# Kernel tuning notes

Measured on AMD Instinct MI355X. Metric: run time of the kernel, lower is better.

Reference implementation:

```python
import jax, jax.numpy as jnp
import numpy as np

H, L, N1, N2, N3 = 256, 141, 9, 34, 98
B, S = 64, 512

def setup_inputs() -> dict:
    key = jax.random.key(0)
    cnt = [0]
    def nrm(shape, s=0.05):
        cnt[0] += 1
        return jax.random.normal(jax.random.fold_in(key, cnt[0]), shape, jnp.float32) * s
    d = {}
    d['inputs'] = jax.random.randint(jax.random.fold_in(key, 1000), (B, S), 0, 30522)
    d['text_hidden'] = nrm((B, S, 768), 1.0)
    d['label_encoding'] = nrm((L, H), 1.0)
    d['w12'] = (jax.random.uniform(jax.random.fold_in(key, 1001), (N1, N2)) < 0.3).astype(jnp.float32)
    d['w23'] = (jax.random.uniform(jax.random.fold_in(key, 1002), (N2, N3)) < 0.3).astype(jnp.float32)
    d['fre12'] = jax.random.uniform(jax.random.fold_in(key, 1003), (N1, N2), jnp.float32)
    d['fre23'] = jax.random.uniform(jax.random.fold_in(key, 1004), (N2, N3), jnp.float32)
    for name in ['wi1', 'wf1', 'wo1', 'wu1', 'wi2', 'wf2', 'wo2', 'wu2']:
        d[name + '_W'] = nrm((H, H)); d[name + '_b'] = nrm((H,))
    for name in ['ui1', 'uf1', 'uo1', 'uu1', 'ui2', 'uf2', 'uo2', 'uu2']:
        d[name + '_W'] = nrm((H, H))
    d['mix_W'] = nrm((3 * H, H)); d['mix_b'] = nrm((H,))
    d['tt_W'] = nrm((768, H)); d['tt_b'] = nrm((H,))
    d['A'] = nrm((L, L)); d['Wp'] = nrm((H, H))
    d['out_W'] = nrm((L * H, L)); d['out_b'] = nrm((L,))
    return d

def reference(inputs, text_hidden, label_encoding, w12, w23, fre12, fre23,
              wi1_W, wi1_b, wf1_W, wf1_b, wo1_W, wo1_b, wu1_W, wu1_b,
              wi2_W, wi2_b, wf2_W, wf2_b, wo2_W, wo2_b, wu2_W, wu2_b,
              ui1_W, uf1_W, uo1_W, uu1_W, ui2_W, uf2_W, uo2_W, uu2_W,
              mix_W, mix_b, tt_W, tt_b, A, Wp, out_W, out_b):
    sig, tanh = jax.nn.sigmoid, jnp.tanh
    v1 = label_encoding[:N1]          # [N1,H]
    v2 = label_encoding[N1:N1 + N2]   # [N2,H]
    v3 = label_encoding[N1 + N2:]     # [N3,H]
    w21, w32 = w12.T, w23.T
    # --- top-down tree-LSTM (suffix 1) ---
    i11 = sig(v1 @ wi1_W + wi1_b); o11 = sig(v1 @ wo1_W + wo1_b); u11 = tanh(v1 @ wu1_W + wu1_b)
    c11 = i11 * u11; h11 = o11 * tanh(c11)
    h21t = w21 @ h11
    i21 = sig(v2 @ wi1_W + wi1_b + h21t @ ui1_W)
    f21 = sig(v2 @ wf1_W + wf1_b + h21t @ uf1_W)
    o21 = sig(v2 @ wo1_W + wo1_b + h21t @ uo1_W)
    u21 = tanh(v2 @ wu1_W + wu1_b + h21t @ uu1_W)
    c21 = i21 * u21 + f21 * (w21 @ c11); h21 = o21 * tanh(c21)
    h31t = w32 @ h21
    i31 = sig(v3 @ wi1_W + wi1_b + h31t @ ui1_W)
    f31 = sig(v3 @ wf1_W + wf1_b + h31t @ uf1_W)
    o31 = sig(v3 @ wo1_W + wo1_b + h31t @ uo1_W)
    u31 = tanh(v3 @ wu1_W + wu1_b + h31t @ uu1_W)
    c31 = i31 * u31 + f31 * (w32 @ c21); h31 = o31 * tanh(c31)
    # --- bottom-up tree-LSTM (suffix 2) ---
    i32 = sig(v3 @ wi2_W + wi2_b); o32 = sig(v3 @ wo2_W + wo2_b); u32 = tanh(v3 @ wu2_W + wu2_b)
    c32 = i32 * u32; h32 = o32 * tanh(c32)
    h22t = fre23 @ h32
    i22 = sig(v2 @ wi2_W + wi2_b + h22t @ ui2_W)
    f22 = sig((w32 @ v2) @ wf2_W + wf2_b + h32 @ uf2_W)   # [N3,H]
    o22 = sig(v2 @ wo2_W + wo2_b + h22t @ uo2_W)
    u22 = tanh(v2 @ wu2_W + wu2_b + h22t @ uu2_W)
    c22 = i22 * u22 + w23 @ (f22 * c32); h22 = o22 * tanh(c22)
    h12t = fre12 @ h22
    i12 = sig(v1 @ wi2_W + wi2_b + h12t @ ui2_W)
    f12 = sig((w21 @ v1) @ wf2_W + wf2_b + h22 @ uf2_W)   # [N2,H]
    o12 = sig(v1 @ wo2_W + wo2_b + h12t @ uo2_W)
    u12 = tanh(v1 @ wu2_W + wu2_b + h12t @ uu2_W)
    c12 = i12 * u12 + w12 @ (f12 * c22); h12 = o12 * tanh(c12)
    h1 = jnp.concatenate([h11, h12], axis=1)
    h2 = jnp.concatenate([h21, h22], axis=1)
    h3 = jnp.concatenate([h31, h32], axis=1)
    le = jnp.concatenate([h1, h2, h3], axis=0)            # [L,2H]
    temp = jax.nn.relu(A @ label_encoding @ Wp)           # [L,H]
    le = jnp.concatenate([le, temp], axis=1) @ mix_W + mix_b  # [L,H]
    # --- masked cross-attention pooling over text ---
    text = tanh(text_hidden @ tt_W + tt_b)                # [B,S,H]
    att = jnp.einsum('lh,bsh->bls', le, text)             # [B,L,S]
    pad = jnp.where((inputs == 0) | (inputs == 101) | (inputs == 102), -jnp.inf, 0.0).astype(text.dtype)
    att = jax.nn.softmax(att + pad[:, None, :], axis=2)
    features = jnp.einsum('bls,bsh->blh', att, text).reshape(inputs.shape[0], -1)  # [B,L*H]
    return sig(features @ out_W + out_b)                  # [B,L]
```

## Files before the change

kernel.cpp:

```cpp
#include <hip/hip_runtime.h>
#include <math.h>

static constexpr int H = 256, L = 141, N1 = 9, N2 = 34, N3 = 98;
static constexpr int B = 64, S = 512;

typedef __attribute__((ext_vector_type(8))) _Float16 f16x8;
typedef __attribute__((ext_vector_type(4))) float f32x4;

__device__ inline unsigned short f2h(float x) {
    _Float16 h = (_Float16)x;
    return __builtin_bit_cast(unsigned short, h);
}
__device__ inline float sigf(float x) { return 1.f / (1.f + __expf(-x)); }

__device__ inline void gload_lds16(const void* g, void* l) {
    __builtin_amdgcn_global_load_lds(
        (const __attribute__((address_space(1))) void*)g,
        (__attribute__((address_space(3))) void*)l, 16, 0, 0);
}

template<int EPI, bool CONVA, int IM>
__global__ __launch_bounds__(256) void gemm_mfma(
    const void* __restrict__ Aptr, int lda, long strA,
    const unsigned short* __restrict__ Bp, int ldb, long strB,
    float* __restrict__ C, int ldc, long strC,
    int M, int N, int K,
    const float* __restrict__ bias,
    const int* __restrict__ tokens,
    unsigned short* __restrict__ outH,
    unsigned short* __restrict__ outHT,
    int kChunk)
{
    __shared__ unsigned short A_s[32 * IM * 32];
    __shared__ unsigned short B_s[128 * 32];
    __shared__ unsigned short T[EPI == 1 ? 128 * 64 : 1];
    const int tid  = threadIdx.x;
    const int wave = tid >> 6, lane = tid & 63;
    const int quad = lane >> 4, l16 = lane & 15;
    const int bz = blockIdx.z;
    const int m0 = blockIdx.y * (32 * IM), n0 = blockIdx.x * 128;
    const int wm = (wave & 1) * (16 * IM), wn = (wave >> 1) * 64;

    long aBase, bBase;
    int kBeg, kEnd;
    if (EPI == 4) { aBase = 0; bBase = 0; kBeg = bz * kChunk; kEnd = kBeg + kChunk; }
    else { aBase = (long)bz * strA; bBase = (long)bz * strB; kBeg = 0; kEnd = K; }

    f32x4 acc[IM][4] = {};

    for (int k0 = kBeg; k0 < kEnd; k0 += 32) {
        if (CONVA) {
            const float* Af = (const float*)Aptr + aBase;
            #pragma unroll
            for (int it = 0; it < IM; it++) {
                int idx = it * 256 + tid;
                int row = idx >> 3, col4 = idx & 7;
                int gm = m0 + row; if (gm > M - 1) gm = M - 1;
                float4 v = *(const float4*)(Af + (long)gm * lda + k0 + col4 * 4);
                unsigned int p0 = f2h(v.x) | ((unsigned int)f2h(v.y) << 16);
                unsigned int p1 = f2h(v.z) | ((unsigned int)f2h(v.w) << 16);
                *(uint2*)&A_s[row * 32 + col4 * 4] = make_uint2(p0, p1);
            }
        } else {
            const unsigned short* Ab = (const unsigned short*)Aptr + aBase;
            #pragma unroll
            for (int t = 0; t < IM / 2; t++) {
                int rowb = wave * (8 * IM) + t * 16;
                int gm = m0 + rowb + (lane >> 2); if (gm > M - 1) gm = M - 1;
                gload_lds16(Ab + (long)gm * lda + k0 + (lane & 3) * 8,
                            &A_s[rowb * 32]);
            }
        }
        #pragma unroll
        for (int t = 0; t < 2; t++) {
            int rowb = wave * 32 + t * 16;
            int gn = n0 + rowb + (lane >> 2); if (gn > N - 1) gn = N - 1;
            gload_lds16(Bp + bBase + (long)gn * ldb + k0 + (lane & 3) * 8,
                        &B_s[rowb * 32]);
        }
        __syncthreads();
        f16x8 a[IM], b[4];
        #pragma unroll
        for (int i = 0; i < IM; i++)
            a[i] = *(const f16x8*)&A_s[(wm + i * 16 + l16) * 32 + quad * 8];
        #pragma unroll
        for (int j = 0; j < 4; j++)
            b[j] = *(const f16x8*)&B_s[(wn + j * 16 + l16) * 32 + quad * 8];
        #pragma unroll
        for (int i = 0; i < IM; i++)
            #pragma unroll
            for (int j = 0; j < 4; j++)
                acc[i][j] = __builtin_amdgcn_mfma_f32_16x16x32_f16(
                    a[i], b[j], acc[i][j], 0, 0, 0);
        __syncthreads();
    }

    #pragma unroll
    for (int i = 0; i < IM; i++) {
        #pragma unroll
        for (int j = 0; j < 4; j++) {
            #pragma unroll
            for (int r = 0; r < 4; r++) {
                int ml = wm + i * 16 + quad * 4 + r;
                int nl = wn + j * 16 + l16;
                int gm = m0 + ml, gn = n0 + nl;
                if (gm >= M || gn >= N) continue;
                float v = acc[i][j][r];
                if (EPI == 1) {
                    v = tanhf(v + bias[gn]);
                    unsigned short hv = f2h(v);
                    outH[(long)gm * ldc + gn] = hv;
                    T[nl * 64 + ml] = hv;
                } else if (EPI == 2) {
                    int tok = tokens[(long)bz * 512 + gn];
                    if (tok == 0 || tok == 101 || tok == 102) v -= 1e30f;
                    C[(long)bz * strC + (long)gm * ldc + gn] = v;
                } else if (EPI == 3) {
                    outH[(long)bz * strC + (long)gm * ldc + gn] = f2h(v);
                } else {
                    C[(long)bz * strC + (long)gm * ldc + gn] = v;
                }
            }
        }
    }
    if (EPI == 1) {
        __syncthreads();
        int bb = m0 >> 9, s0 = m0 & 511;
        int rr = tid >> 1, half = tid & 1;
        const uint4* srcp = (const uint4*)&T[rr * 64 + half * 32];
        uint4* dstp = (uint4*)&outHT[((long)bb * 256 + n0 + rr) * 512 + s0 + half * 32];
        dstp[0] = srcp[0]; dstp[1] = srcp[1]; dstp[2] = srcp[2]; dstp[3] = srcp[3];
    }
}

__global__ __launch_bounds__(256) void transp_t64(
    const float* __restrict__ src, unsigned short* __restrict__ dst,
    int R, int C)
{
    __shared__ unsigned short T[64 * 65];
    const int tid = threadIdx.x;
    const int r0 = blockIdx.x * 64, c0 = blockIdx.y * 64;
    #pragma unroll
    for (int p = 0; p < 16; p++) {
        int lin = p * 256 + tid;
        int r = lin >> 6, c = lin & 63;
        int gc = c0 + c;
        float v = (gc < C) ? src[(long)(r0 + r) * C + gc] : 0.f;
        T[c * 65 + r] = f2h(v);
    }
    __syncthreads();
    #pragma unroll
    for (int p = 0; p < 16; p++) {
        int lin = p * 256 + tid;
        int c = lin >> 6, r = lin & 63;
        if (c0 + c < C)
            dst[(long)(c0 + c) * R + r0 + r] = T[c * 65 + r];
    }
}

__global__ __launch_bounds__(256) void gate_pre(
    const float* __restrict__ le,
    const float* W0, const float* W1, const float* W2, const float* W3,
    const float* W4, const float* W5, const float* W6,
    const float* b0, const float* b1, const float* b2, const float* b3,
    const float* b4, const float* b5, const float* b6,
    float* __restrict__ G)
{
    __shared__ float ls[256];
    __shared__ float red[256];
    const int j = blockIdx.x >> 2, x = blockIdx.x & 3, m = blockIdx.y;
    const int tid = threadIdx.x, nl = tid & 63, ks = tid >> 6, n = x * 64 + nl;
    ls[tid] = le[(long)m * 256 + tid];
    __syncthreads();
    const float *W, *bb;
    switch (j) {
        case 0: W = W0; bb = b0; break;  case 1: W = W1; bb = b1; break;
        case 2: W = W2; bb = b2; break;  case 3: W = W3; bb = b3; break;
        case 4: W = W4; bb = b4; break;  case 5: W = W5; bb = b5; break;
        default: W = W6; bb = b6;
    }
    float a0 = 0, a1 = 0, a2 = 0, a3 = 0;
    for (int k = ks; k + 12 < 256; k += 16) {
        long o = (long)k * 256 + n;
        a0 += ls[k] * W[o];        a1 += ls[k + 4] * W[o + 1024];
        a2 += ls[k + 8] * W[o + 2048]; a3 += ls[k + 12] * W[o + 3072];
    }
    red[tid] = a0 + a1 + a2 + a3;
    __syncthreads();
    if (ks == 0)
        G[((long)j * 141 + m) * 256 + n] =
            red[nl] + red[64 + nl] + red[128 + nl] + red[192 + nl] + bb[n];
}

__global__ __launch_bounds__(256) void pre2(
    const float* __restrict__ A, const float* __restrict__ le,
    const float* __restrict__ w23, const float* __restrict__ w12,
    const float* __restrict__ Wp, const float* __restrict__ wf2_W,
    float* __restrict__ tmpP, float* __restrict__ wv2f, float* __restrict__ wv1f)
{
    __shared__ float cs[141];
    __shared__ float t[256];
    __shared__ float red[256];
    const int x = blockIdx.x, y = blockIdx.y;
    const int tid = threadIdx.x, nl = tid & 63, ks = tid >> 6, n = x * 64 + nl;
    int job, m, K1;
    if (y < 141)      { job = 0; m = y;       K1 = 141; }
    else if (y < 239) { job = 1; m = y - 141; K1 = 34; }
    else              { job = 2; m = y - 239; K1 = 9; }
    if (tid < K1)
        cs[tid] = (job == 0) ? A[(long)m * 141 + tid]
                : (job == 1) ? w23[(long)tid * 98 + m]
                             : w12[(long)tid * 34 + m];
    __syncthreads();
    const float* s1 = (job == 1) ? le + 9 * 256 : le;
    float acc = 0;
    #pragma unroll 4
    for (int k = 0; k < K1; k++) acc += cs[k] * s1[(long)k * 256 + tid];
    t[tid] = acc;
    __syncthreads();
    const float* W = (job == 0) ? Wp : wf2_W;
    float a0 = 0, a1 = 0, a2 = 0, a3 = 0;
    for (int k = ks; k + 12 < 256; k += 16) {
        long o = (long)k * 256 + n;
        a0 += t[k] * W[o];        a1 += t[k + 4] * W[o + 1024];
        a2 += t[k + 8] * W[o + 2048]; a3 += t[k + 12] * W[o + 3072];
    }
    red[tid] = a0 + a1 + a2 + a3;
    __syncthreads();
    if (ks == 0) {
        float tot = red[nl] + red[64 + nl] + red[128 + nl] + red[192 + nl];
        if (job == 0)      tmpP[(long)m * 256 + n] = fmaxf(tot, 0.f);
        else if (job == 1) wv2f[(long)m * 256 + n] = tot;
        else               wv1f[(long)m * 256 + n] = tot;
    }
}

__global__ __launch_bounds__(256) void ew1(
    const float* __restrict__ G, float* __restrict__ h11, float* __restrict__ c11,
    float* __restrict__ h32, float* __restrict__ c32)
{
    int y = blockIdx.x, n = threadIdx.x;
    if (y < 9) {
        int m = y;
        float iv = sigf(G[(0L * 141 + m) * 256 + n]);
        float ov = sigf(G[(2L * 141 + m) * 256 + n]);
        float uv = tanhf(G[(3L * 141 + m) * 256 + n]);
        float cv = iv * uv;
        c11[m * 256 + n] = cv; h11[m * 256 + n] = ov * tanhf(cv);
    } else {
        int r = y - 9, grow = 43 + r;
        float iv = sigf(G[(4L * 141 + grow) * 256 + n]);
        float ov = sigf(G[(5L * 141 + grow) * 256 + n]);
        float uv = tanhf(G[(6L * 141 + grow) * 256 + n]);
        float cv = iv * uv;
        c32[r * 256 + n] = cv; h32[r * 256 + n] = ov * tanhf(cv);
    }
}

__global__ __launch_bounds__(256) void chain_mm(int phase,
    const float* __restrict__ w12, const float* __restrict__ w23,
    const float* __restrict__ fre23, const float* __restrict__ fre12,
    const float* __restrict__ h11, const float* __restrict__ c11,
    const float* __restrict__ h32,
    const float* __restrict__ h21, const float* __restrict__ c21,
    const float* __restrict__ h22,
    const float* __restrict__ wv2f, const float* __restrict__ wv1f,
    const float* __restrict__ wf2_b, const float* __restrict__ uf2_W,
    const float* __restrict__ c32, const float* __restrict__ c22,
    float* __restrict__ h21t, float* __restrict__ c21p,
    float* __restrict__ h22t, float* __restrict__ fcb,
    float* __restrict__ h31t, float* __restrict__ c31p,
    float* __restrict__ h12t, float* __restrict__ fc2b)
{
    __shared__ float cs[256];
    __shared__ float red[256];
    const int x = blockIdx.x, y = blockIdx.y;
    const int tid = threadIdx.x, nl = tid & 63, ks = tid >> 6, n = x * 64 + nl;
    int job, m;
    if (phase == 0) {
        if (y < 34)       { job = 0; m = y; }
        else if (y < 68)  { job = 1; m = y - 34; }
        else if (y < 102) { job = 2; m = y - 68; }
        else              { job = 3; m = y - 102; }
    } else {
        if (y < 98)       { job = 0; m = y; }
        else if (y < 196) { job = 1; m = y - 98; }
        else if (y < 205) { job = 2; m = y - 196; }
        else              { job = 3; m = y - 205; }
    }
    if (job < 3) {
        int K; const float* src; float* dst;
        if (phase == 0) {
            K = (job == 2) ? 98 : 9;
            src = (job == 0) ? h11 : (job == 1) ? c11 : h32;
            dst = (job == 0) ? h21t : (job == 1) ? c21p : h22t;
            if (tid < K)
                cs[tid] = (job == 2) ? fre23[(long)m * 98 + tid]
                                     : w12[(long)tid * 34 + m];
        } else {
            K = 34;
            src = (job == 0) ? h21 : (job == 1) ? c21 : h22;
            dst = (job == 0) ? h31t : (job == 1) ? c31p : h12t;
            if (tid < K)
                cs[tid] = (job == 2) ? fre12[(long)m * 34 + tid]
                                     : w23[(long)tid * 98 + m];
        }
        __syncthreads();
        float a0 = 0;
        for (int k = ks; k < K; k += 4) a0 += cs[k] * src[(long)k * 256 + n];
        red[tid] = a0;
        __syncthreads();
        if (ks == 0)
            dst[(long)m * 256 + n] = red[nl] + red[64 + nl] + red[128 + nl] + red[192 + nl];
    } else {
        const float* row = (phase == 0) ? h32 + m * 256 : h22 + m * 256;
        const float* pre = (phase == 0) ? wv2f : wv1f;
        const float* cm  = (phase == 0) ? c32 : c22;
        float* dst       = (phase == 0) ? fcb : fc2b;
        cs[tid] = row[tid];
        __syncthreads();
        float a0 = 0, a1 = 0, a2 = 0, a3 = 0;
        for (int k = ks; k + 12 < 256; k += 16) {
            long o = (long)k * 256 + n;
            a0 += cs[k] * uf2_W[o];        a1 += cs[k + 4] * uf2_W[o + 1024];
            a2 += cs[k + 8] * uf2_W[o + 2048]; a3 += cs[k + 12] * uf2_W[o + 3072];
        }
        red[tid] = a0 + a1 + a2 + a3;
        __syncthreads();
        if (ks == 0) {
            float tot = red[nl] + red[64 + nl] + red[128 + nl] + red[192 + nl]
                      + pre[(long)m * 256 + n] + wf2_b[n];
            dst[(long)m * 256 + n] = sigf(tot) * cm[(long)m * 256 + n];
        }
    }
}

__global__ __launch_bounds__(256) void lstm_fused(int phase,
    const float* __restrict__ G,
    const float* __restrict__ h21t, const float* __restrict__ c21p,
    const float* __restrict__ h22t, const float* __restrict__ fcb,
    const float* __restrict__ h31t, const float* __restrict__ c31p,
    const float* __restrict__ h12t, const float* __restrict__ fc2b,
    const float* __restrict__ w23, const float* __restrict__ w12,
    const float* __restrict__ ui1, const float* __restrict__ uf1,
    const float* __restrict__ uo1, const float* __restrict__ uu1,
    const float* __restrict__ ui2, const float* __restrict__ uo2,
    const float* __restrict__ uu2,
    float* __restrict__ h21, float* __restrict__ c21,
    float* __restrict__ h22, float* __restrict__ c22,
    float* __restrict__ h31, float* __restrict__ h12)
{
    __shared__ float hs[256];
    __shared__ float cs[128];
    __shared__ float red[1024];
    const int x = blockIdx.x, y = blockIdx.y;
    const int tid = threadIdx.x, nl = tid & 63, ks = tid >> 6, n = x * 64 + nl;
    bool modef; int m, grow, Kx = 0;
    const float *hrow, *U0, *U1, *U2, *U3 = nullptr, *Sx = nullptr, *cmod = nullptr;
    float *ho, *co = nullptr;
    if (phase == 0) {
        if (y < 34) { modef = true;  m = y;      grow = 9 + m;  hrow = h21t;
                      U0 = ui1; U1 = uf1; U2 = uo1; U3 = uu1; cmod = c21p; ho = h21; co = c21; }
        else        { modef = false; m = y - 34; grow = 9 + m;  hrow = h22t;
                      U0 = ui2; U1 = uo2; U2 = uu2; Sx = fcb; Kx = 98; ho = h22; co = c22;
                      if (tid < 98) cs[tid] = w23[(long)m * 98 + tid]; }
    } else {
        if (y < 98) { modef = true;  m = y;      grow = 43 + m; hrow = h31t;
                      U0 = ui1; U1 = uf1; U2 = uo1; U3 = uu1; cmod = c31p; ho = h31; co = nullptr; }
        else        { modef = false; m = y - 98; grow = m;      hrow = h12t;
                      U0 = ui2; U1 = uo2; U2 = uu2; Sx = fc2b; Kx = 34; ho = h12; co = nullptr;
                      if (tid < 34) cs[tid] = w12[(long)m * 34 + tid]; }
    }
    hs[tid] = hrow[(long)m * 256 + tid];
    __syncthreads();
    float a0 = 0, a1 = 0, a2 = 0, a3 = 0;
    if (modef) {
        for (int k = ks; k < 256; k += 4) {
            float xv = hs[k]; long o = (long)k * 256 + n;
            a0 += xv * U0[o]; a1 += xv * U1[o]; a2 += xv * U2[o]; a3 += xv * U3[o];
        }
    } else {
        for (int k = ks; k < 256; k += 4) {
            float xv = hs[k]; long o = (long)k * 256 + n;
            a0 += xv * U0[o]; a1 += xv * U1[o]; a2 += xv * U2[o];
        }
        for (int k = ks; k < Kx; k += 4) a3 += cs[k] * Sx[(long)k * 256 + n];
    }
    red[tid] = a0; red[256 + tid] = a1; red[512 + tid] = a2; red[768 + tid] = a3;
    __syncthreads();
    if (ks == 0) {
        float t0 = 0, t1 = 0, t2 = 0, t3 = 0;
        #pragma unroll
        for (int s2 = 0; s2 < 4; s2++) {
            t0 += red[s2 * 64 + nl];       t1 += red[256 + s2 * 64 + nl];
            t2 += red[512 + s2 * 64 + nl]; t3 += red[768 + s2 * 64 + nl];
        }
        if (modef) {
            float ti = t0 + G[(0L * 141 + grow) * 256 + n];
            float tf = t1 + G[(1L * 141 + grow) * 256 + n];
            float to = t2 + G[(2L * 141 + grow) * 256 + n];
            float tu = t3 + G[(3L * 141 + grow) * 256 + n];
            float cv = sigf(ti) * tanhf(tu) + sigf(tf) * cmod[(long)m * 256 + n];
            ho[(long)m * 256 + n] = sigf(to) * tanhf(cv);
            if (co) co[(long)m * 256 + n] = cv;
        } else {
            float ti = t0 + G[(4L * 141 + grow) * 256 + n];
            float to = t1 + G[(5L * 141 + grow) * 256 + n];
            float tu = t2 + G[(6L * 141 + grow) * 256 + n];
            float cv = sigf(ti) * tanhf(tu) + t3;
            ho[(long)m * 256 + n] = sigf(to) * tanhf(cv);
            if (co) co[(long)m * 256 + n] = cv;
        }
    }
}

__global__ __launch_bounds__(256) void mix_mm(
    const float* __restrict__ h11, const float* __restrict__ h12,
    const float* __restrict__ h21, const float* __restrict__ h22,
    const float* __restrict__ h31, const float* __restrict__ h32,
    const float* __restrict__ tmpP, const float* __restrict__ mix_W,
    const float* __restrict__ mix_b, unsigned short* __restrict__ le_h)
{
    __shared__ float ls[768];
    __shared__ float red[256];
    const int x = blockIdx.x, l = blockIdx.y;
    const int tid = threadIdx.x, nl = tid & 63, ks = tid >> 6, n = x * 64 + nl;
    const float *pa, *pb; int r;
    if (l < 9)       { pa = h11; pb = h12; r = l; }
    else if (l < 43) { pa = h21; pb = h22; r = l - 9; }
    else             { pa = h31; pb = h32; r = l - 43; }
    for (int j = tid; j < 768; j += 256) {
        float v;
        if (j < 256)      v = pa[r * 256 + j];
        else if (j < 512) v = pb[r * 256 + (j - 256)];
        else              v = tmpP[l * 256 + (j - 512)];
        ls[j] = v;
    }
    __syncthreads();
    float a0 = 0, a1 = 0, a2 = 0, a3 = 0;
    for (int k = ks; k + 12 < 768; k += 16) {
        long o = (long)k * 256 + n;
        a0 += ls[k] * mix_W[o];        a1 += ls[k + 4] * mix_W[o + 1024];
        a2 += ls[k + 8] * mix_W[o + 2048]; a3 += ls[k + 12] * mix_W[o + 3072];
    }
    red[tid] = a0 + a1 + a2 + a3;
    __syncthreads();
    if (ks == 0) {
        float tot = red[nl] + red[64 + nl] + red[128 + nl] + red[192 + nl] + mix_b[n];
        le_h[(long)l * 256 + n] = f2h(tot);
    }
}

__global__ __launch_bounds__(256) void softmax512(
    const float* __restrict__ att, unsigned short* __restrict__ atth)
{
    __shared__ float red[256];
    const float* row = att + (long)blockIdx.x * 512;
    unsigned short* orow = atth + (long)blockIdx.x * 512;
    int t = threadIdx.x;
    float a = row[t], b = row[t + 256];
    red[t] = fmaxf(a, b);
    __syncthreads();
    for (int s = 128; s > 0; s >>= 1) {
        if (t < s) red[t] = fmaxf(red[t], red[t + s]);
        __syncthreads();
    }
    float m = red[0];
    __syncthreads();
    float ea = __expf(a - m), eb = __expf(b - m);
    red[t] = ea + eb;
    __syncthreads();
    for (int s = 128; s > 0; s >>= 1) {
        if (t < s) red[t] += red[t + s];
        __syncthreads();
    }
    float inv = 1.f / red[0];
    orow[t] = f2h(ea * inv);
    orow[t + 256] = f2h(eb * inv);
}

__global__ __launch_bounds__(256) void out_final(
    const float* __restrict__ acc, const float* __restrict__ ob,
    float* __restrict__ out, int total, int nz)
{
    int i = blockIdx.x * 256 + threadIdx.x;
    if (i >= total) return;
    float v = ob[i % L];
    #pragma unroll 4
    for (int z = 0; z < nz; z++) v += acc[(long)z * total + i];
    out[i] = sigf(v);
}

extern "C" void kernel_launch(void* const* d_in, const int* in_sizes, int n_in,
                              void* d_out, int out_size, void* d_ws, size_t ws_size,
                              hipStream_t stream)
{
    (void)in_sizes; (void)n_in; (void)out_size; (void)ws_size;
    const int*   inputs      = (const int*)d_in[0];
    const float* text_hidden = (const float*)d_in[1];
    const float* label_enc   = (const float*)d_in[2];
    const float* w12   = (const float*)d_in[3];
    const float* w23   = (const float*)d_in[4];
    const float* fre12 = (const float*)d_in[5];
    const float* fre23 = (const float*)d_in[6];
    const float* wi1_W = (const float*)d_in[7],  *wi1_b = (const float*)d_in[8];
    const float* wf1_W = (const float*)d_in[9],  *wf1_b = (const float*)d_in[10];
    const float* wo1_W = (const float*)d_in[11], *wo1_b = (const float*)d_in[12];
    const float* wu1_W = (const float*)d_in[13], *wu1_b = (const float*)d_in[14];
    const float* wi2_W = (const float*)d_in[15], *wi2_b = (const float*)d_in[16];
    const float* wf2_W = (const float*)d_in[17], *wf2_b = (const float*)d_in[18];
    const float* wo2_W = (const float*)d_in[19], *wo2_b = (const float*)d_in[20];
    const float* wu2_W = (const float*)d_in[21], *wu2_b = (const float*)d_in[22];
    const float* ui1_W = (const float*)d_in[23], *uf1_W = (const float*)d_in[24];
    const float* uo1_W = (const float*)d_in[25], *uu1_W = (const float*)d_in[26];
    const float* ui2_W = (const float*)d_in[27], *uf2_W = (const float*)d_in[28];
    const float* uo2_W = (const float*)d_in[29], *uu2_W = (const float*)d_in[30];
    const float* mix_W = (const float*)d_in[31], *mix_b = (const float*)d_in[32];
    const float* tt_W  = (const float*)d_in[33], *tt_b  = (const float*)d_in[34];
    const float* Amat  = (const float*)d_in[35], *Wp    = (const float*)d_in[36];
    const float* out_W = (const float*)d_in[37], *out_b = (const float*)d_in[38];
    float* out = (float*)d_out;

    float* ws = (float*)d_ws;
    float* att     = ws; ws += (long)B * L * S;
    unsigned short* text_h  = (unsigned short*)ws; ws += (long)B * S * H / 2;
    unsigned short* text_hT = (unsigned short*)ws; ws += (long)B * S * H / 2;
    unsigned short* att_h   = (unsigned short*)ws; ws += (long)B * L * S / 2;
    unsigned short* tt_Wt   = (unsigned short*)ws; ws += 768 * H / 2;
    unsigned short* le_h    = (unsigned short*)ws; ws += L * H / 2 + 4;
    unsigned short* out_Wh  = (unsigned short*)ws; ws += (long)L * 36096 / 2;
    unsigned short* feat_h  = (unsigned short*)ws; ws += (long)B * L * H / 2;
    float* outacc = ws; ws += (long)B * L * 141;
    float* G    = ws; ws += 7 * 141 * 256;
    float* tmpP = ws; ws += L * H;
    float* wv2f = ws; ws += N3 * H;
    float* wv1f = ws; ws += N2 * H;
    float* h11  = ws; ws += N1 * H;  float* c11  = ws; ws += N1 * H;
    float* h21  = ws; ws += N2 * H;  float* c21  = ws; ws += N2 * H;
    float* h21t = ws; ws += N2 * H;  float* c21p = ws; ws += N2 * H;
    float* h31  = ws; ws += N3 * H;  float* h31t = ws; ws += N3 * H;
    float* c31p = ws; ws += N3 * H;
    float* h32  = ws; ws += N3 * H;  float* c32  = ws; ws += N3 * H;
    float* h22  = ws; ws += N2 * H;  float* c22  = ws; ws += N2 * H;
    float* h22t = ws; ws += N2 * H;  float* fcb  = ws; ws += N3 * H;
    float* h12  = ws; ws += N1 * H;  float* h12t = ws; ws += N1 * H;
    float* fc2b = ws; ws += N2 * H;

    transp_t64<<<dim3(768 / 64, 256 / 64), 256, 0, stream>>>(tt_W, tt_Wt, 768, 256);
    gemm_mfma<1, true, 2><<<dim3(H / 128, (B * S) / 64, 1), 256, 0, stream>>>(
        text_hidden, 768, 0, tt_Wt, 768, 0, nullptr, H, 0,
        B * S, H, 768, tt_b, nullptr, text_h, text_hT, 0);
    gate_pre<<<dim3(28, 141), 256, 0, stream>>>(label_enc,
        wi1_W, wf1_W, wo1_W, wu1_W, wi2_W, wo2_W, wu2_W,
        wi1_b, wf1_b, wo1_b, wu1_b, wi2_b, wo2_b, wu2_b, G);
    pre2<<<dim3(4, 273), 256, 0, stream>>>(Amat, label_enc, w23, w12, Wp, wf2_W,
        tmpP, wv2f, wv1f);
    transp_t64<<<dim3(36096 / 64, 3), 256, 0, stream>>>(out_W, out_Wh, 36096, 141);
    ew1<<<107, 256, 0, stream>>>(G, h11, c11, h32, c32);
    chain_mm<<<dim3(4, 200), 256, 0, stream>>>(0, w12, w23, fre23, fre12,
        h11, c11, h32, h21, c21, h22, wv2f, wv1f, wf2_b, uf2_W, c32, c22,
        h21t, c21p, h22t, fcb, h31t, c31p, h12t, fc2b);
    lstm_fused<<<dim3(4, 68), 256, 0, stream>>>(0, G,
        h21t, c21p, h22t, fcb, h31t, c31p, h12t, fc2b, w23, w12,
        ui1_W, uf1_W, uo1_W, uu1_W, ui2_W, uo2_W, uu2_W,
        h21, c21, h22, c22, h31, h12);
    chain_mm<<<dim3(4, 239), 256, 0, stream>>>(1, w12, w23, fre23, fre12,
        h11, c11, h32, h21, c21, h22, wv2f, wv1f, wf2_b, uf2_W, c32, c22,
        h21t, c21p, h22t, fcb, h31t, c31p, h12t, fc2b);
    lstm_fused<<<dim3(4, 107), 256, 0, stream>>>(1, G,
        h21t, c21p, h22t, fcb, h31t, c31p, h12t, fc2b, w23, w12,
        ui1_W, uf1_W, uo1_W, uu1_W, ui2_W, uo2_W, uu2_W,
        h21, c21, h22, c22, h31, h12);
    mix_mm<<<dim3(4, 141), 256, 0, stream>>>(h11, h12, h21, h22, h31, h32,
        tmpP, mix_W, mix_b, le_h);
    gemm_mfma<2, false, 2><<<dim3(S / 128, (L + 63) / 64, B), 256, 0, stream>>>(
        le_h, H, 0, text_h, H, (long)S * H, att, S, (long)L * S,
        L, S, H, nullptr, inputs, nullptr, nullptr, 0);
    softmax512<<<B * L, 256, 0, stream>>>(att, att_h);
    gemm_mfma<3, false, 2><<<dim3(H / 128, (L + 63) / 64, B), 256, 0, stream>>>(
        att_h, S, (long)L * S, text_hT, S, (long)H * S, nullptr, H, (long)L * H,
        L, H, S, nullptr, nullptr, feat_h, nullptr, 0);
    gemm_mfma<4, false, 2><<<dim3(2, 1, 141), 256, 0, stream>>>(
        feat_h, L * H, 0, out_Wh, L * H, 0, outacc, L, (long)B * L,
        B, L, L * H, nullptr, nullptr, nullptr, nullptr, 256);
    out_final<<<(B * L + 255) / 256, 256, 0, stream>>>(outacc, out_b, out, B * L, 141);
}
```

Baseline: 486.0 us.

## Add double-buffered specialized text projection GEMM with register-prefetched fp32 A

Replaces the generic templated MFMA GEMM for the text projection (B*S x 768 x 256, tanh epilogue plus transposed fp16 output) with a dedicated kernel. The new kernel double-buffers the A and B tiles in LDS, prefetching fp32 A two steps ahead into registers and streaming B via global-to-LDS loads, so memory latency overlaps the MFMA work. It uses a single barrier per K step and hardcoded dimensions. The cost is more LDS and more registers per block, which may lower occupancy.

```diff
diff --git a/kernel.cpp b/kernel.cpp
--- a/kernel.cpp
+++ b/kernel.cpp
@@ -17,6 +17,134 @@
     __builtin_amdgcn_global_load_lds(
         (const __attribute__((address_space(1))) void*)g,
         (__attribute__((address_space(3))) void*)l, 16, 0, 0);
+}
+
+__device__ inline void cvt_store8(unsigned short* buf, int off, float4 v) {
+    unsigned int p0 = f2h(v.x) | ((unsigned int)f2h(v.y) << 16);
+    unsigned int p1 = f2h(v.z) | ((unsigned int)f2h(v.w) << 16);
+    *(uint2*)&buf[off] = make_uint2(p0, p1);
+}
+
+__global__ __launch_bounds__(256) void text_gemm(
+    const float* __restrict__ Af,
+    const unsigned short* __restrict__ Bh,
+    const float* __restrict__ bias,
+    unsigned short* __restrict__ outH,
+    unsigned short* __restrict__ outHT)
+{
+    __shared__ unsigned short A_s[2][64 * 32];
+    __shared__ unsigned short B_s[2][128 * 32];
+    __shared__ unsigned short T[128 * 64];
+    const int tid  = threadIdx.x;
+    const int wave = tid >> 6, lane = tid & 63;
+    const int quad = lane >> 4, l16 = lane & 15;
+    const int m0 = blockIdx.y * 64, n0 = blockIdx.x * 128;
+    const int wm = (wave & 1) * 32, wn = (wave >> 1) * 64;
+    constexpr int NT = 24;
+
+    const int arow0 = tid >> 3;
+    const int acol4 = tid & 7;
+    const float* aptr0 = Af + (long)(m0 + arow0) * 768 + acol4 * 4;
+    const float* aptr1 = Af + (long)(m0 + 32 + arow0) * 768 + acol4 * 4;
+    const int c16w = acol4 >> 1, low8 = acol4 & 1;
+    const int awoff0 = arow0 * 32 + ((c16w ^ (arow0 & 3)) * 8) + low8 * 4;
+    const int awoff1 = (arow0 + 32) * 32 + ((c16w ^ (arow0 & 3)) * 8) + low8 * 4;
+
+    const int bchunk = (lane & 3) ^ ((lane >> 2) & 3);
+    const int brow0 = wave * 32 + (lane >> 2);
+    const unsigned short* bptr0 = Bh + (long)(n0 + brow0) * 768 + bchunk * 8;
+    const unsigned short* bptr1 = bptr0 + (long)16 * 768;
+    const int bdst0 = (wave * 32) * 32, bdst1 = (wave * 32 + 16) * 32;
+
+    int aro[2], bro[4];
+    #pragma unroll
+    for (int i = 0; i < 2; i++) {
+        int r = wm + i * 16 + l16;
+        aro[i] = r * 32 + (quad ^ (r & 3)) * 8;
+    }
+    #pragma unroll
+    for (int j = 0; j < 4; j++) {
+        int r = wn + j * 16 + l16;
+        bro[j] = r * 32 + (quad ^ (r & 3)) * 8;
+    }
+
+    f32x4 acc[2][4] = {};
+    float4 areg[2];
+
+    areg[0] = *(const float4*)aptr0;
+    areg[1] = *(const float4*)aptr1;
+    gload_lds16(bptr0, &B_s[0][bdst0]);
+    gload_lds16(bptr1, &B_s[0][bdst1]);
+    cvt_store8(A_s[0], awoff0, areg[0]);
+    cvt_store8(A_s[0], awoff1, areg[1]);
+    areg[0] = *(const float4*)(aptr0 + 32);
+    areg[1] = *(const float4*)(aptr1 + 32);
+    asm volatile("s_waitcnt vmcnt(2)" ::: "memory");
+    asm volatile("s_waitcnt lgkmcnt(0)" ::: "memory");
+    __builtin_amdgcn_s_barrier();
+    gload_lds16(bptr0 + 32, &B_s[1][bdst0]);
+    gload_lds16(bptr1 + 32, &B_s[1][bdst1]);
+
+    int cur = 0;
+    #pragma unroll 1
+    for (int t = 0; t < NT; t++) {
+        f16x8 a[2], b[4];
+        #pragma unroll
+        for (int i = 0; i < 2; i++) a[i] = *(const f16x8*)&A_s[cur][aro[i]];
+        #pragma unroll
+        for (int j = 0; j < 4; j++) b[j] = *(const f16x8*)&B_s[cur][bro[j]];
+        if (t + 1 < NT) {
+            cvt_store8(A_s[cur ^ 1], awoff0, areg[0]);
+            cvt_store8(A_s[cur ^ 1], awoff1, areg[1]);
+        }
+        if (t + 2 < NT) {
+            areg[0] = *(const float4*)(aptr0 + (t + 2) * 32);
+            areg[1] = *(const float4*)(aptr1 + (t + 2) * 32);
+        }
+        #pragma unroll
+        for (int i = 0; i < 2; i++)
+            #pragma unroll
+            for (int j = 0; j < 4; j++)
+                acc[i][j] = __builtin_amdgcn_mfma_f32_16x16x32_f16(
+                    a[i], b[j], acc[i][j], 0, 0, 0);
+        if (t + 1 < NT) {
+            if (t + 2 < NT) {
+                asm volatile("s_waitcnt vmcnt(2)" ::: "memory");
+            } else {
+                asm volatile("s_waitcnt vmcnt(0)" ::: "memory");
+            }
+            asm volatile("s_waitcnt lgkmcnt(0)" ::: "memory");
+            __builtin_amdgcn_s_barrier();
+            cur ^= 1;
+            if (t + 2 < NT) {
+                gload_lds16(bptr0 + (t + 2) * 32, &B_s[cur ^ 1][bdst0]);
+                gload_lds16(bptr1 + (t + 2) * 32, &B_s[cur ^ 1][bdst1]);
+            }
+        }
+    }
+
+    #pragma unroll
+    for (int i = 0; i < 2; i++) {
+        #pragma unroll
+        for (int j = 0; j < 4; j++) {
+            #pragma unroll
+            for (int r = 0; r < 4; r++) {
+                int ml = wm + i * 16 + quad * 4 + r;
+                int nl = wn + j * 16 + l16;
+                int gm = m0 + ml, gn = n0 + nl;
+                float v = tanhf(acc[i][j][r] + bias[gn]);
+                unsigned short hv = f2h(v);
+                outH[(long)gm * 256 + gn] = hv;
+                T[nl * 64 + ml] = hv;
+            }
+        }
+    }
+    __syncthreads();
+    int bb = m0 >> 9, s0 = m0 & 511;
+    int rr = tid >> 1, half = tid & 1;
+    const uint4* srcp = (const uint4*)&T[rr * 64 + half * 32];
+    uint4* dstp = (uint4*)&outHT[((long)bb * 256 + n0 + rr) * 512 + s0 + half * 32];
+    dstp[0] = srcp[0]; dstp[1] = srcp[1]; dstp[2] = srcp[2]; dstp[3] = srcp[3];
 }
 
 template<int EPI, bool CONVA, int IM>
@@ -547,9 +675,8 @@
     float* fc2b = ws; ws += N2 * H;
 
     transp_t64<<<dim3(768 / 64, 256 / 64), 256, 0, stream>>>(tt_W, tt_Wt, 768, 256);
-    gemm_mfma<1, true, 2><<<dim3(H / 128, (B * S) / 64, 1), 256, 0, stream>>>(
-        text_hidden, 768, 0, tt_Wt, 768, 0, nullptr, H, 0,
-        B * S, H, 768, tt_b, nullptr, text_h, text_hT, 0);
+    text_gemm<<<dim3(2, 512), 256, 0, stream>>>(
+        text_hidden, tt_Wt, tt_b, text_h, text_hT);
     gate_pre<<<dim3(28, 141), 256, 0, stream>>>(label_enc,
         wi1_W, wf1_W, wo1_W, wu1_W, wi2_W, wo2_W, wu2_W,
         wi1_b, wf1_b, wo1_b, wu1_b, wi2_b, wo2_b, wu2_b, G);
```

New measurement: 475.2 us. 2.2% less time.

## Replace text projection GEMM with register-fed MFMA kernel and prepacked fp16 weights

Applied to the files above, without the earlier changes.

Swaps the generic LDS-staged MFMA GEMM for the tanh(text_hidden @ tt_W + tt_b) projection for a dedicated kernel. Each block computes a full 64x256 output tile, so the fp32 activations are read only once instead of once per 128-column tile. A and B fragments are loaded straight into registers with double buffering, skipping the LDS staging. A new conversion kernel prepacks tt_W into a k-chunked fp16 layout suited to direct fragment loads, and the transposed output is written through an LDS tile. Risks include higher register pressure from the large accumulator and register buffers, and uncoalesced strided A loads.

```diff
diff --git a/kernel.cpp b/kernel.cpp
--- a/kernel.cpp
+++ b/kernel.cpp
@@ -17,6 +17,122 @@
     __builtin_amdgcn_global_load_lds(
         (const __attribute__((address_space(1))) void*)g,
         (__attribute__((address_space(3))) void*)l, 16, 0, 0);
+}
+
+__device__ inline f16x8 cvt8(float4 lo, float4 hi) {
+    union { unsigned int u[4]; f16x8 v; } r;
+    r.u[0] = f2h(lo.x) | ((unsigned int)f2h(lo.y) << 16);
+    r.u[1] = f2h(lo.z) | ((unsigned int)f2h(lo.w) << 16);
+    r.u[2] = f2h(hi.x) | ((unsigned int)f2h(hi.y) << 16);
+    r.u[3] = f2h(hi.z) | ((unsigned int)f2h(hi.w) << 16);
+    return r.v;
+}
+
+__global__ __launch_bounds__(256) void conv_ttW(
+    const float* __restrict__ W, unsigned short* __restrict__ Bt)
+{
+    __shared__ unsigned short Tl[32][257];
+    const int t = blockIdx.x, tid = threadIdx.x;
+    #pragma unroll
+    for (int p = 0; p < 32; p++) {
+        int lin = p * 256 + tid;
+        int r = lin >> 8, c = lin & 255;
+        Tl[r][c] = f2h(W[(long)(t * 32 + r) * 256 + c]);
+    }
+    __syncthreads();
+    unsigned short v[32];
+    #pragma unroll
+    for (int kin = 0; kin < 32; kin++) v[kin] = Tl[kin][tid];
+    uint4* dst = (uint4*)(Bt + ((long)t * 256 + tid) * 32);
+    #pragma unroll
+    for (int q = 0; q < 4; q++) dst[q] = ((const uint4*)v)[q];
+}
+
+__global__ __launch_bounds__(256) void text_gemm2(
+    const float* __restrict__ Af,
+    const unsigned short* __restrict__ Bt,
+    const float* __restrict__ bias,
+    unsigned short* __restrict__ outH,
+    unsigned short* __restrict__ outHT)
+{
+    __shared__ unsigned short T[256 * 72];
+    const int tid  = threadIdx.x;
+    const int wave = tid >> 6, lane = tid & 63;
+    const int quad = lane >> 4, l16 = lane & 15;
+    const int m0 = blockIdx.x * 64;
+    const int wm = (wave & 1) * 32;
+    const int wn = (wave >> 1) * 128;
+
+    const float* ap0 = Af + (long)(m0 + wm + l16) * 768 + quad * 8;
+    const float* ap1 = ap0 + 16 * 768;
+    const unsigned short* bp = Bt + (wn + l16) * 32 + quad * 8;
+
+    f32x4 acc[2][8] = {};
+    uint4  br0[8], br1[8];
+    float4 ar0[4], ar1[4];
+
+    auto tg_load = [&](int tt, uint4 (&BR)[8], float4 (&AR)[4]) {
+        const unsigned short* bq = bp + (long)tt * 8192;
+        #pragma unroll
+        for (int j = 0; j < 8; j++) BR[j] = *(const uint4*)(bq + j * 512);
+        const float* a0 = ap0 + tt * 32;
+        const float* a1 = ap1 + tt * 32;
+        AR[0] = *(const float4*)a0;
+        AR[1] = *(const float4*)(a0 + 4);
+        AR[2] = *(const float4*)a1;
+        AR[3] = *(const float4*)(a1 + 4);
+    };
+    auto tg_comp = [&](const uint4 (&BR)[8], const float4 (&AR)[4]) {
+        f16x8 a0 = cvt8(AR[0], AR[1]);
+        f16x8 a1 = cvt8(AR[2], AR[3]);
+        #pragma unroll
+        for (int j = 0; j < 8; j++) {
+            f16x8 bj = __builtin_bit_cast(f16x8, BR[j]);
+            acc[0][j] = __builtin_amdgcn_mfma_f32_16x16x32_f16(a0, bj, acc[0][j], 0, 0, 0);
+            acc[1][j] = __builtin_amdgcn_mfma_f32_16x16x32_f16(a1, bj, acc[1][j], 0, 0, 0);
+        }
+    };
+
+    tg_load(0, br0, ar0);
+    #pragma unroll 1
+    for (int t = 0; t < 24; t += 2) {
+        tg_load(t + 1, br1, ar1);
+        tg_comp(br0, ar0);
+        if (t + 2 < 24) tg_load(t + 2, br0, ar0);
+        tg_comp(br1, ar1);
+    }
+
+    float bv[8];
+    #pragma unroll
+    for (int j = 0; j < 8; j++) bv[j] = bias[wn + j * 16 + l16];
+
+    #pragma unroll
+    for (int i = 0; i < 2; i++) {
+        #pragma unroll
+        for (int j = 0; j < 8; j++) {
+            const int mlb = wm + i * 16 + quad * 4;
+            const int n   = wn + j * 16 + l16;
+            unsigned short hv[4];
+            #pragma unroll
+            for (int r = 0; r < 4; r++) {
+                float v = tanhf(acc[i][j][r] + bv[j]);
+                hv[r] = f2h(v);
+                outH[(long)(m0 + mlb + r) * 256 + n] = hv[r];
+            }
+            uint2 p;
+            p.x = hv[0] | ((unsigned int)hv[1] << 16);
+            p.y = hv[2] | ((unsigned int)hv[3] << 16);
+            *(uint2*)&T[n * 72 + mlb] = p;
+        }
+    }
+    __syncthreads();
+    {
+        const int bb = m0 >> 9, s0 = m0 & 511;
+        uint4* dst = (uint4*)&outHT[((long)bb * 256 + tid) * 512 + s0];
+        const uint4* src = (const uint4*)&T[tid * 72];
+        #pragma unroll
+        for (int q = 0; q < 8; q++) dst[q] = src[q];
+    }
 }
 
 template<int EPI, bool CONVA, int IM>
@@ -546,10 +662,9 @@
     float* h12  = ws; ws += N1 * H;  float* h12t = ws; ws += N1 * H;
     float* fc2b = ws; ws += N2 * H;
 
-    transp_t64<<<dim3(768 / 64, 256 / 64), 256, 0, stream>>>(tt_W, tt_Wt, 768, 256);
-    gemm_mfma<1, true, 2><<<dim3(H / 128, (B * S) / 64, 1), 256, 0, stream>>>(
-        text_hidden, 768, 0, tt_Wt, 768, 0, nullptr, H, 0,
-        B * S, H, 768, tt_b, nullptr, text_h, text_hT, 0);
+    conv_ttW<<<24, 256, 0, stream>>>(tt_W, tt_Wt);
+    text_gemm2<<<512, 256, 0, stream>>>(
+        text_hidden, tt_Wt, tt_b, text_h, text_hT);
     gate_pre<<<dim3(28, 141), 256, 0, stream>>>(label_enc,
         wi1_W, wf1_W, wo1_W, wu1_W, wi2_W, wo2_W, wu2_W,
         wi1_b, wf1_b, wo1_b, wu1_b, wi2_b, wo2_b, wu2_b, G);
```

After: 482.0 us. No clear change (-0.8%).
